# Performance work log

Hardware: AMD Instinct MI355X
Metric: run time of the kernel (lower is better)

Reference implementation:

```python
import jax, jax.numpy as jnp
import numpy as np

B, S, DIM = 2, 2048, 1024
N_HEAD, HEAD_DIM = 16, 64


def setup_inputs() -> dict:
    key = jax.random.key(0)
    k1, k2, k3, k4 = jax.random.split(key, 4)
    x = jax.random.normal(k1, (B, S, DIM), dtype=jnp.float32)
    # rotary table: cos/sin pairs, shape [S, head_dim//2, 2]
    half = HEAD_DIM // 2
    inv_freq = 1.0 / (10000.0 ** (jnp.arange(0, half, dtype=jnp.float32) / half))
    t = jnp.arange(S, dtype=jnp.float32)
    ang = t[:, None] * inv_freq[None, :]
    freqs_cis = jnp.stack([jnp.cos(ang), jnp.sin(ang)], axis=-1)  # [S, half, 2]
    # causal boolean mask [1,1,S,S] (True = attend)
    mask = jnp.tril(jnp.ones((S, S), dtype=bool))[None, None]
    wqkv = jax.random.normal(k2, (3 * DIM, DIM), dtype=jnp.float32) * (DIM ** -0.5)
    wo = jax.random.normal(k3, (DIM, DIM), dtype=jnp.float32) * (DIM ** -0.5)
    return {"x": x, "freqs_cis": freqs_cis, "mask": mask, "wqkv": wqkv, "wo": wo}


def apply_rotary_emb(x, freqs_cis):
    # x: [B, S, H, D]; freqs_cis: [S, D//2, 2]
    xs = x.reshape(*x.shape[:-1], -1, 2)  # [B,S,H,D//2,2]
    fc = freqs_cis[None, :, None, :, :]  # [1,S,1,D//2,2]
    xr, xi = xs[..., 0], xs[..., 1]
    cr, ci = fc[..., 0], fc[..., 1]
    out = jnp.stack([xr * cr - xi * ci, xi * cr + xr * ci], axis=-1)
    return out.reshape(x.shape)


def reference(x, freqs_cis, mask, wqkv, wo):
    bsz, seqlen, _ = x.shape
    qkv = jnp.einsum('bsd,ed->bse', x, wqkv)  # [B,S,3*dim]
    q, k, v = jnp.split(qkv, 3, axis=-1)
    q = q.reshape(bsz, seqlen, N_HEAD, HEAD_DIM)
    k = k.reshape(bsz, seqlen, N_HEAD, HEAD_DIM)
    v = v.reshape(bsz, seqlen, N_HEAD, HEAD_DIM)
    q = apply_rotary_emb(q, freqs_cis)
    k = apply_rotary_emb(k, freqs_cis)
    scale = HEAD_DIM ** -0.5
    scores = jnp.einsum('bqhd,bkhd->bhqk', q, k) * scale  # [B,H,S,S]
    scores = jnp.where(mask, scores, jnp.finfo(scores.dtype).min)
    attn = jax.nn.softmax(scores, axis=-1)
    y = jnp.einsum('bhqk,bkhd->bqhd', attn, v).reshape(bsz, seqlen, N_HEAD * HEAD_DIM)
    return jnp.einsum('bse,de->bsd', y, wo)
```

## Files before the change

kernel.cpp:

```cpp
#include <hip/hip_runtime.h>
#include <hip/hip_bf16.h>
#include <stdint.h>


typedef __attribute__((ext_vector_type(8))) __bf16 bf16x8;
typedef __attribute__((ext_vector_type(4))) float f32x4;

union B8 { uint4 u; bf16x8 v; unsigned short us[8]; };

static __device__ __forceinline__ float bf2f(unsigned short u) {
  union { unsigned int ui; float f; } x; x.ui = ((unsigned int)u) << 16; return x.f;
}
static __device__ __forceinline__ unsigned short f2bf(float f) {
  union { float f; unsigned int ui; } x; x.f = f;
  unsigned int r = x.ui + 0x7fffu + ((x.ui >> 16) & 1u);
  return (unsigned short)(r >> 16);
}
static __device__ __forceinline__ f32x4 mfma16(bf16x8 a, bf16x8 b, f32x4 c) {
  return __builtin_amdgcn_mfma_f32_16x16x32_bf16(a, b, c, 0, 0, 0);
}
#define AS1 __attribute__((address_space(1)))
#define AS3 __attribute__((address_space(3)))
static __device__ __forceinline__ void gload_lds16(const void* g, void* l) {
  __builtin_amdgcn_global_load_lds((const AS1 unsigned int*)g,
                                   (AS3 unsigned int*)l, 16, 0, 0);
}

__global__ __launch_bounds__(256) void cvt_all_kernel(
    const float* __restrict__ x, const float* __restrict__ wqkv,
    const float* __restrict__ wo,
    unsigned short* __restrict__ xb, unsigned short* __restrict__ wqkvb,
    unsigned short* __restrict__ wob) {
  int i = blockIdx.x * 256 + threadIdx.x;
  const float* src; unsigned short* dst; int off;
  if (i < 1048576)       { src = x;    dst = xb;    off = i; }
  else if (i < 1835008)  { src = wqkv; dst = wqkvb; off = i - 1048576; }
  else                   { src = wo;   dst = wob;   off = i - 1835008; }
  float4 f = ((const float4*)src)[off];
  ushort4 u;
  u.x = f2bf(f.x); u.y = f2bf(f.y); u.z = f2bf(f.z); u.w = f2bf(f.w);
  ((ushort4*)dst)[off] = u;
}

__global__ __launch_bounds__(256) void qkv_rope_kernel(
    const unsigned short* __restrict__ xb,
    const unsigned short* __restrict__ wqkvb,
    const float* __restrict__ freqs,
    unsigned short* __restrict__ Q,
    unsigned short* __restrict__ K,
    unsigned short* __restrict__ Vt)
{
  __shared__ __align__(16) unsigned short As[128 * 64];
  __shared__ __align__(16) unsigned short Bs[128 * 64];
  const int t = threadIdx.x;
  const int lane = t & 63, wv = t >> 6;
  const int c = lane & 15, quad = lane >> 4;
  const int wm = wv >> 1, wn = wv & 1;
  const int tm = blockIdx.x & 31, tn = blockIdx.x >> 5;
  const int m0 = tm * 128, n0 = tn * 128;

  f32x4 acc[4][4] = {};

  for (int k0 = 0; k0 < 1024; k0 += 64) {
    for (int r = 0; r < 4; ++r) {
      int cid = t + 256 * r;
      int row = cid >> 3, jc = cid & 7;
      int sc = jc ^ (row & 7);
      gload_lds16(xb    + (size_t)(m0 + row) * 1024 + k0 + sc * 8, (char*)As + cid * 16);
      gload_lds16(wqkvb + (size_t)(n0 + row) * 1024 + k0 + sc * 8, (char*)Bs + cid * 16);
    }
    __syncthreads();
    for (int ks = 0; ks < 2; ++ks) {
      bf16x8 a[4], b[4];
      for (int st = 0; st < 4; ++st) {
        int ra = wm * 64 + st * 16 + c;
        int sa = (ks * 4 + quad) ^ (ra & 7);
        a[st] = *(const bf16x8*)((const char*)As + ra * 128 + sa * 16);
        int rb = wn * 64 + st * 16 + c;
        int sb = (ks * 4 + quad) ^ (rb & 7);
        b[st] = *(const bf16x8*)((const char*)Bs + rb * 128 + sb * 16);
      }
      for (int sm = 0; sm < 4; ++sm)
        for (int sn = 0; sn < 4; ++sn)
          acc[sm][sn] = mfma16(a[sm], b[sn], acc[sm][sn]);
    }
    __syncthreads();
  }

  for (int sm = 0; sm < 4; ++sm) {
    for (int sn = 0; sn < 4; ++sn) {
      const int e = n0 + wn * 64 + sn * 16 + c;
      const int seg = e >> 10;
      const int eh = e & 1023;
      const int h = eh >> 6, d = eh & 63;
      for (int i = 0; i < 4; ++i) {
        const int m = m0 + wm * 64 + sm * 16 + quad * 4 + i;
        const int b_ = m >> 11, s_ = m & 2047;
        float v = acc[sm][sn][i];
        if (seg == 2) {
          Vt[((size_t)(b_ * 16 + h) * 64 + d) * 2048 + s_] = f2bf(v);
        } else {
          float partner = __shfl_xor(v, 1, 64);
          const int p = d >> 1;
          float cr = freqs[s_ * 64 + p * 2];
          float ci = freqs[s_ * 64 + p * 2 + 1];
          float outv = (d & 1) ? (v * cr + partner * ci) : (v * cr - partner * ci);
          unsigned short* dst = (seg == 0) ? Q : K;
          dst[((size_t)(b_ * 16 + h) * 2048 + s_) * 64 + d] = f2bf(outv);
        }
      }
    }
  }
}

struct QState {
  bf16x8 qf0, qf1;
  f32x4 o[4];
  float lp[4];
};

static __device__ __forceinline__ void attn_chunk(
    QState& st, const char* Ks, const char* Vs, float* myp,
    int c, int quad, int k0, int q0, bool diag)
{
  f32x4 sfr[4];
  for (int kc = 0; kc < 4; ++kc) {
    const int key = kc * 16 + c;
    const int s0 = quad ^ (key & 7), s1 = (4 + quad) ^ (key & 7);
    f32x4 sacc = {};
    sacc = mfma16(st.qf0, *(const bf16x8*)(Ks + key * 128 + s0 * 16), sacc);
    sacc = mfma16(st.qf1, *(const bf16x8*)(Ks + key * 128 + s1 * 16), sacc);
    sfr[kc] = sacc;
  }
  for (int i = 0; i < 4; ++i) {
    const int qrow = q0 + quad * 4 + i;
    float e[4];
    for (int kc = 0; kc < 4; ++kc) {
      float arg = fmaf(sfr[kc][i], 0.18033688f, -20.19773057f);
      if (diag && (k0 + kc * 16 + c > qrow)) arg = -1e30f;
      e[kc] = exp2f(arg);
    }
    st.lp[i] += (e[0] + e[1]) + (e[2] + e[3]);
    const int prow = (quad * 4 + i) * 68;
    myp[prow + c]      = e[0];
    myp[prow + 16 + c] = e[1];
    myp[prow + 32 + c] = e[2];
    myp[prow + 48 + c] = e[3];
  }
  bf16x8 pf[2];
  for (int sH = 0; sH < 2; ++sH) {
    const float* src = myp + c * 68 + sH * 32 + quad * 8;
    float4 f0 = *(const float4*)(src);
    float4 f1 = *(const float4*)(src + 4);
    B8 p;
    p.us[0] = f2bf(f0.x); p.us[1] = f2bf(f0.y);
    p.us[2] = f2bf(f0.z); p.us[3] = f2bf(f0.w);
    p.us[4] = f2bf(f1.x); p.us[5] = f2bf(f1.y);
    p.us[6] = f2bf(f1.z); p.us[7] = f2bf(f1.w);
    pf[sH] = p.v;
  }
  for (int ct = 0; ct < 4; ++ct) {
    const int d = ct * 16 + c;
    const int s0 = quad ^ (d & 7), s1 = (4 + quad) ^ (d & 7);
    st.o[ct] = mfma16(pf[0], *(const bf16x8*)(Vs + d * 128 + s0 * 16), st.o[ct]);
    st.o[ct] = mfma16(pf[1], *(const bf16x8*)(Vs + d * 128 + s1 * 16), st.o[ct]);
  }
}

__global__ __launch_bounds__(256) void attn_partial_kernel(
    const unsigned short* __restrict__ Q,
    const unsigned short* __restrict__ K,
    const unsigned short* __restrict__ Vt,
    unsigned short* __restrict__ Po,
    float* __restrict__ Pl)
{
  __shared__ __align__(16) unsigned short Ks[64 * 64];
  __shared__ __align__(16) unsigned short Vs[64 * 64];
  __shared__ __align__(16) float plds[4][16 * 68];
  const int t = threadIdx.x;
  const int lane = t & 63, wv = t >> 6;
  const int c = lane & 15, quad = lane >> 4;
  const int bh = blockIdx.x & 31;
  const int rest = blockIdx.x >> 5;
  const int j = rest >> 1, half = rest & 1;
  const int qA = j * 64 + wv * 16;
  const int qB = (31 - j) * 64 + wv * 16;

  const unsigned short* Qb = Q + (size_t)bh * (2048 * 64);
  const unsigned short* Kb = K + (size_t)bh * (2048 * 64);
  const unsigned short* Vb = Vt + (size_t)bh * (64 * 2048);

  QState A = {}, Bst = {};
  A.qf0 = *(const bf16x8*)(Qb + (qA + c) * 64 + quad * 8);
  A.qf1 = *(const bf16x8*)(Qb + (qA + c) * 64 + 32 + quad * 8);
  Bst.qf0 = *(const bf16x8*)(Qb + (qB + c) * 64 + quad * 8);
  Bst.qf1 = *(const bf16x8*)(Qb + (qB + c) * 64 + 32 + quad * 8);

  float* myp = plds[wv];
  const int ktmax = 31 - j;

  for (int kt = half; kt <= ktmax; kt += 2) {
    const int k0 = kt * 64;
    __syncthreads();
    for (int r = 0; r < 2; ++r) {
      int cid = t + 256 * r;
      int row = cid >> 3, jc = cid & 7;
      int sc = jc ^ (row & 7);
      gload_lds16(Kb + (size_t)(k0 + row) * 64 + sc * 8, (char*)Ks + cid * 16);
      gload_lds16(Vb + (size_t)row * 2048 + k0 + sc * 8, (char*)Vs + cid * 16);
    }
    __syncthreads();
    attn_chunk(Bst, (const char*)Ks, (const char*)Vs, myp, c, quad,
               k0, qB, kt == ktmax);
    if (kt <= j)
      attn_chunk(A, (const char*)Ks, (const char*)Vs, myp, c, quad,
                 k0, qA, kt == j);
  }

  unsigned short* Poh = Po + (size_t)half * (32 * 2048 * 64) + (size_t)bh * (2048 * 64);
  float* Plh = Pl + (size_t)half * (32 * 2048) + bh * 2048;
  for (int set = 0; set < 2; ++set) {
    QState& st = set ? Bst : A;
    const int q0 = set ? qB : qA;
    for (int i = 0; i < 4; ++i) {
      float l = st.lp[i];
      l += __shfl_xor(l, 1, 16);
      l += __shfl_xor(l, 2, 16);
      l += __shfl_xor(l, 4, 16);
      l += __shfl_xor(l, 8, 16);
      const int s = q0 + quad * 4 + i;
      for (int ct = 0; ct < 4; ++ct)
        Poh[(size_t)s * 64 + ct * 16 + c] = f2bf(st.o[ct][i]);
      if (c == 0) Plh[s] = l;
    }
  }
}

__global__ __launch_bounds__(256) void combine_kernel(
    const unsigned short* __restrict__ Po, const float* __restrict__ Pl,
    unsigned short* __restrict__ Yb)
{
  const int idx = blockIdx.x * 256 + threadIdx.x;
  const int bh = idx >> 14, rem = idx & 16383;
  const int s = rem >> 3, g = rem & 7;
  const size_t base = (size_t)bh * (2048 * 64) + (size_t)s * 64 + g * 8;
  B8 a, b;
  a.u = *(const uint4*)(Po + base);
  b.u = *(const uint4*)(Po + (size_t)(32 * 2048 * 64) + base);
  float l = Pl[bh * 2048 + s] + Pl[32 * 2048 + bh * 2048 + s];
  float inv = 1.0f / l;
  B8 y;
  for (int k = 0; k < 8; ++k)
    y.us[k] = f2bf((bf2f(a.us[k]) + bf2f(b.us[k])) * inv);
  const int b_ = bh >> 4, h = bh & 15;
  *(uint4*)(Yb + ((size_t)(b_ * 2048 + s)) * 1024 + h * 64 + g * 8) = y.u;
}

__global__ __launch_bounds__(256) void attn_kernel(
    const unsigned short* __restrict__ Q,
    const unsigned short* __restrict__ K,
    const unsigned short* __restrict__ Vt,
    unsigned short* __restrict__ Y)
{
  __shared__ __align__(16) unsigned short Ks[64 * 64];
  __shared__ __align__(16) unsigned short Vs[64 * 64];
  __shared__ __align__(16) float plds[4][16 * 68];
  const int t = threadIdx.x;
  const int lane = t & 63, wv = t >> 6;
  const int c = lane & 15, quad = lane >> 4;
  const int j = blockIdx.x >> 5, bh = blockIdx.x & 31;
  const int b = bh >> 4, h = bh & 15;
  const int qA = j * 64 + wv * 16;
  const int qB = (31 - j) * 64 + wv * 16;

  const unsigned short* Qb = Q + (size_t)bh * (2048 * 64);
  const unsigned short* Kb = K + (size_t)bh * (2048 * 64);
  const unsigned short* Vb = Vt + (size_t)bh * (64 * 2048);

  QState A = {}, Bst = {};
  A.qf0 = *(const bf16x8*)(Qb + (qA + c) * 64 + quad * 8);
  A.qf1 = *(const bf16x8*)(Qb + (qA + c) * 64 + 32 + quad * 8);
  Bst.qf0 = *(const bf16x8*)(Qb + (qB + c) * 64 + quad * 8);
  Bst.qf1 = *(const bf16x8*)(Qb + (qB + c) * 64 + 32 + quad * 8);

  const int nkt = 32 - j;
  float* myp = plds[wv];

  for (int kt = 0; kt < nkt; ++kt) {
    const int k0 = kt * 64;
    __syncthreads();
    for (int r = 0; r < 2; ++r) {
      int cid = t + 256 * r;
      int row = cid >> 3, jc = cid & 7;
      int sc = jc ^ (row & 7);
      gload_lds16(Kb + (size_t)(k0 + row) * 64 + sc * 8, (char*)Ks + cid * 16);
      gload_lds16(Vb + (size_t)row * 2048 + k0 + sc * 8, (char*)Vs + cid * 16);
    }
    __syncthreads();
    attn_chunk(Bst, (const char*)Ks, (const char*)Vs, myp, c, quad,
               k0, qB, kt == 31 - j);
    if (kt <= j)
      attn_chunk(A, (const char*)Ks, (const char*)Vs, myp, c, quad,
                 k0, qA, kt == j);
  }

  for (int set = 0; set < 2; ++set) {
    QState& st = set ? Bst : A;
    const int q0 = set ? qB : qA;
    for (int i = 0; i < 4; ++i) {
      float l = st.lp[i];
      l += __shfl_xor(l, 1, 16);
      l += __shfl_xor(l, 2, 16);
      l += __shfl_xor(l, 4, 16);
      l += __shfl_xor(l, 8, 16);
      float inv = 1.0f / l;
      const int s = q0 + quad * 4 + i;
      unsigned short* dst = Y + ((size_t)(b * 2048 + s)) * 1024 + h * 64;
      for (int ct = 0; ct < 4; ++ct)
        dst[ct * 16 + c] = f2bf(st.o[ct][i] * inv);
    }
  }
}

__global__ __launch_bounds__(256) void out_proj_kernel(
    const unsigned short* __restrict__ Y,
    const unsigned short* __restrict__ wob,
    float* __restrict__ out)
{
  __shared__ __align__(16) unsigned short As[64 * 64];
  __shared__ __align__(16) unsigned short Bs[64 * 64];
  const int t = threadIdx.x;
  const int lane = t & 63, wv = t >> 6;
  const int c = lane & 15, quad = lane >> 4;
  const int wm = wv >> 1, wn = wv & 1;
  const int tm = blockIdx.x & 63, tn = blockIdx.x >> 6;
  const int m0 = tm * 64, n0 = tn * 64;

  f32x4 acc[2][2] = {};

  for (int k0 = 0; k0 < 1024; k0 += 64) {
    for (int r = 0; r < 2; ++r) {
      int cid = t + 256 * r;
      int row = cid >> 3, jc = cid & 7;
      int sc = jc ^ (row & 7);
      gload_lds16(Y   + (size_t)(m0 + row) * 1024 + k0 + sc * 8, (char*)As + cid * 16);
      gload_lds16(wob + (size_t)(n0 + row) * 1024 + k0 + sc * 8, (char*)Bs + cid * 16);
    }
    __syncthreads();
    for (int ks = 0; ks < 2; ++ks) {
      bf16x8 a[2], b[2];
      for (int st = 0; st < 2; ++st) {
        int ra = wm * 32 + st * 16 + c;
        int sa = (ks * 4 + quad) ^ (ra & 7);
        a[st] = *(const bf16x8*)((const char*)As + ra * 128 + sa * 16);
        int rb = wn * 32 + st * 16 + c;
        int sb = (ks * 4 + quad) ^ (rb & 7);
        b[st] = *(const bf16x8*)((const char*)Bs + rb * 128 + sb * 16);
      }
      for (int sm = 0; sm < 2; ++sm)
        for (int sn = 0; sn < 2; ++sn)
          acc[sm][sn] = mfma16(a[sm], b[sn], acc[sm][sn]);
    }
    __syncthreads();
  }

  for (int sm = 0; sm < 2; ++sm)
    for (int sn = 0; sn < 2; ++sn)
      for (int i = 0; i < 4; ++i) {
        const int m = m0 + wm * 32 + sm * 16 + quad * 4 + i;
        const int e = n0 + wn * 32 + sn * 16 + c;
        out[(size_t)m * 1024 + e] = acc[sm][sn][i];
      }
}

extern "C" void kernel_launch(void* const* d_in, const int* in_sizes, int n_in,
                              void* d_out, int out_size, void* d_ws, size_t ws_size,
                              hipStream_t stream) {
  const float* x     = (const float*)d_in[0];
  const float* freqs = (const float*)d_in[1];
  const float* wqkv  = (const float*)d_in[3];
  const float* wo    = (const float*)d_in[4];
  float* out = (float*)d_out;

  const size_t BHSD = (size_t)2 * 16 * 2048 * 64;
  unsigned short* Q     = (unsigned short*)d_ws;
  unsigned short* K     = Q + BHSD;
  unsigned short* Vt    = K + BHSD;
  unsigned short* Yb    = Vt + BHSD;
  unsigned short* xb    = Yb + BHSD;
  unsigned short* wqkvb = xb + 4194304;
  unsigned short* wob   = wqkvb + 3145728;
  unsigned short* Po    = wob + 1048576;
  float*          Pl    = (float*)(Po + 2 * BHSD);

  const size_t need_fast =
      (size_t)((char*)(Pl + 2 * 32 * 2048) - (char*)d_ws);

  cvt_all_kernel<<<8192, 256, 0, stream>>>(x, wqkv, wo, xb, wqkvb, wob);
  qkv_rope_kernel<<<768, 256, 0, stream>>>(xb, wqkvb, freqs, Q, K, Vt);
  if (ws_size >= need_fast) {
    attn_partial_kernel<<<1024, 256, 0, stream>>>(Q, K, Vt, Po, Pl);
    combine_kernel<<<2048, 256, 0, stream>>>(Po, Pl, Yb);
  } else {
    attn_kernel<<<512, 256, 0, stream>>>(Q, K, Vt, Yb);
  }
  out_proj_kernel<<<1024, 256, 0, stream>>>(Yb, wob, out);
}
```

Before: 229.0 us.

## Use 32x32 MFMA in QKV GEMM, fuse split-KV combine into out-projection, double attention work per block

The QKV projection GEMM switches from 16x16x32 to 32x32x16 bf16 MFMA tiles, with a new lane mapping for the RoPE epilogue. The attention partial kernel now processes two query-block pairs per workgroup, halving the grid and reusing each loaded K/V tile across four query states. The separate combine kernel is removed: its normalise-and-sum of the two split-KV partials is folded into the A-tile load of a new out-projection kernel. This saves a launch and the round trip of the intermediate Y tensor, but the A operand is now loaded through registers rather than direct-to-LDS, and the attention grid has fewer, longer workgroups.

```diff
diff --git a/kernel.cpp b/kernel.cpp
--- a/kernel.cpp
+++ b/kernel.cpp
@@ -5,6 +5,7 @@
 
 typedef __attribute__((ext_vector_type(8))) __bf16 bf16x8;
 typedef __attribute__((ext_vector_type(4))) float f32x4;
+typedef __attribute__((ext_vector_type(16))) float f32x16;
 
 union B8 { uint4 u; bf16x8 v; unsigned short us[8]; };
 
@@ -18,6 +19,9 @@
 }
 static __device__ __forceinline__ f32x4 mfma16(bf16x8 a, bf16x8 b, f32x4 c) {
   return __builtin_amdgcn_mfma_f32_16x16x32_bf16(a, b, c, 0, 0, 0);
+}
+static __device__ __forceinline__ f32x16 mfma32(bf16x8 a, bf16x8 b, f32x16 c) {
+  return __builtin_amdgcn_mfma_f32_32x32x16_bf16(a, b, c, 0, 0, 0);
 }
 #define AS1 __attribute__((address_space(1)))
 #define AS3 __attribute__((address_space(3)))
@@ -54,12 +58,12 @@
   __shared__ __align__(16) unsigned short Bs[128 * 64];
   const int t = threadIdx.x;
   const int lane = t & 63, wv = t >> 6;
-  const int c = lane & 15, quad = lane >> 4;
+  const int l31 = lane & 31, lh = lane >> 5;
   const int wm = wv >> 1, wn = wv & 1;
   const int tm = blockIdx.x & 31, tn = blockIdx.x >> 5;
   const int m0 = tm * 128, n0 = tn * 128;
 
-  f32x4 acc[4][4] = {};
+  f32x16 acc[2][2] = {};
 
   for (int k0 = 0; k0 < 1024; k0 += 64) {
     for (int r = 0; r < 4; ++r) {
@@ -70,40 +74,38 @@
       gload_lds16(wqkvb + (size_t)(n0 + row) * 1024 + k0 + sc * 8, (char*)Bs + cid * 16);
     }
     __syncthreads();
-    for (int ks = 0; ks < 2; ++ks) {
-      bf16x8 a[4], b[4];
-      for (int st = 0; st < 4; ++st) {
-        int ra = wm * 64 + st * 16 + c;
-        int sa = (ks * 4 + quad) ^ (ra & 7);
-        a[st] = *(const bf16x8*)((const char*)As + ra * 128 + sa * 16);
-        int rb = wn * 64 + st * 16 + c;
-        int sb = (ks * 4 + quad) ^ (rb & 7);
-        b[st] = *(const bf16x8*)((const char*)Bs + rb * 128 + sb * 16);
-      }
-      for (int sm = 0; sm < 4; ++sm)
-        for (int sn = 0; sn < 4; ++sn)
-          acc[sm][sn] = mfma16(a[sm], b[sn], acc[sm][sn]);
-    }
-    __syncthreads();
-  }
-
-  for (int sm = 0; sm < 4; ++sm) {
-    for (int sn = 0; sn < 4; ++sn) {
-      const int e = n0 + wn * 64 + sn * 16 + c;
+    for (int kst = 0; kst < 4; ++kst) {
+      const int g = kst * 2 + lh;
+      bf16x8 a[2], b[2];
+      for (int s2 = 0; s2 < 2; ++s2) {
+        int ra = wm * 64 + s2 * 32 + l31;
+        a[s2] = *(const bf16x8*)((const char*)As + ra * 128 + (g ^ (ra & 7)) * 16);
+        int rb = wn * 64 + s2 * 32 + l31;
+        b[s2] = *(const bf16x8*)((const char*)Bs + rb * 128 + (g ^ (rb & 7)) * 16);
+      }
+      for (int sm = 0; sm < 2; ++sm)
+        for (int sn = 0; sn < 2; ++sn)
+          acc[sm][sn] = mfma32(a[sm], b[sn], acc[sm][sn]);
+    }
+    __syncthreads();
+  }
+
+  for (int sm = 0; sm < 2; ++sm) {
+    for (int sn = 0; sn < 2; ++sn) {
+      const int e = n0 + wn * 64 + sn * 32 + l31;
       const int seg = e >> 10;
       const int eh = e & 1023;
       const int h = eh >> 6, d = eh & 63;
-      for (int i = 0; i < 4; ++i) {
-        const int m = m0 + wm * 64 + sm * 16 + quad * 4 + i;
+      for (int r = 0; r < 16; ++r) {
+        const int m = m0 + wm * 64 + sm * 32 + (r & 3) + 8 * (r >> 2) + 4 * lh;
         const int b_ = m >> 11, s_ = m & 2047;
-        float v = acc[sm][sn][i];
+        float v = acc[sm][sn][r];
         if (seg == 2) {
           Vt[((size_t)(b_ * 16 + h) * 64 + d) * 2048 + s_] = f2bf(v);
         } else {
           float partner = __shfl_xor(v, 1, 64);
-          const int p = d >> 1;
-          float cr = freqs[s_ * 64 + p * 2];
-          float ci = freqs[s_ * 64 + p * 2 + 1];
+          float cr = freqs[s_ * 64 + (d & ~1)];
+          float ci = freqs[s_ * 64 + (d | 1)];
           float outv = (d & 1) ? (v * cr + partner * ci) : (v * cr - partner * ci);
           unsigned short* dst = (seg == 0) ? Q : K;
           dst[((size_t)(b_ * 16 + h) * 2048 + s_) * 64 + d] = f2bf(outv);
@@ -118,6 +120,12 @@
   f32x4 o[4];
   float lp[4];
 };
+
+static __device__ __forceinline__ void load_q(QState& st,
+    const unsigned short* Qb, int q0, int c, int quad) {
+  st.qf0 = *(const bf16x8*)(Qb + (q0 + c) * 64 + quad * 8);
+  st.qf1 = *(const bf16x8*)(Qb + (q0 + c) * 64 + 32 + quad * 8);
+}
 
 static __device__ __forceinline__ void attn_chunk(
     QState& st, const char* Ks, const char* Vs, float* myp,
@@ -167,6 +175,23 @@
   }
 }
 
+static __device__ __forceinline__ void write_state(
+    QState& st, int q0, int c, int quad,
+    unsigned short* Poh, float* Plh)
+{
+  for (int i = 0; i < 4; ++i) {
+    float l = st.lp[i];
+    l += __shfl_xor(l, 1, 16);
+    l += __shfl_xor(l, 2, 16);
+    l += __shfl_xor(l, 4, 16);
+    l += __shfl_xor(l, 8, 16);
+    const int s = q0 + quad * 4 + i;
+    for (int ct = 0; ct < 4; ++ct)
+      Poh[(size_t)s * 64 + ct * 16 + c] = f2bf(st.o[ct][i]);
+    if (c == 0) Plh[s] = l;
+  }
+}
+
 __global__ __launch_bounds__(256) void attn_partial_kernel(
     const unsigned short* __restrict__ Q,
     const unsigned short* __restrict__ K,
@@ -181,23 +206,24 @@
   const int lane = t & 63, wv = t >> 6;
   const int c = lane & 15, quad = lane >> 4;
   const int bh = blockIdx.x & 31;
-  const int rest = blockIdx.x >> 5;
-  const int j = rest >> 1, half = rest & 1;
-  const int qA = j * 64 + wv * 16;
-  const int qB = (31 - j) * 64 + wv * 16;
+  const int rr = blockIdx.x >> 5;
+  const int k8 = rr >> 1, half = rr & 1;
+  const int j0 = 2 * k8, j1 = 2 * k8 + 1;
+  const int qA0 = j0 * 64 + wv * 16,  qB0 = (31 - j0) * 64 + wv * 16;
+  const int qA1 = j1 * 64 + wv * 16,  qB1 = (31 - j1) * 64 + wv * 16;
 
   const unsigned short* Qb = Q + (size_t)bh * (2048 * 64);
   const unsigned short* Kb = K + (size_t)bh * (2048 * 64);
   const unsigned short* Vb = Vt + (size_t)bh * (64 * 2048);
 
-  QState A = {}, Bst = {};
-  A.qf0 = *(const bf16x8*)(Qb + (qA + c) * 64 + quad * 8);
-  A.qf1 = *(const bf16x8*)(Qb + (qA + c) * 64 + 32 + quad * 8);
-  Bst.qf0 = *(const bf16x8*)(Qb + (qB + c) * 64 + quad * 8);
-  Bst.qf1 = *(const bf16x8*)(Qb + (qB + c) * 64 + 32 + quad * 8);
+  QState A0 = {}, A1 = {}, B0 = {}, B1 = {};
+  load_q(A0, Qb, qA0, c, quad);
+  load_q(A1, Qb, qA1, c, quad);
+  load_q(B0, Qb, qB0, c, quad);
+  load_q(B1, Qb, qB1, c, quad);
 
   float* myp = plds[wv];
-  const int ktmax = 31 - j;
+  const int ktmax = 31 - j0;
 
   for (int kt = half; kt <= ktmax; kt += 2) {
     const int k0 = kt * 64;
@@ -210,50 +236,25 @@
       gload_lds16(Vb + (size_t)row * 2048 + k0 + sc * 8, (char*)Vs + cid * 16);
     }
     __syncthreads();
-    attn_chunk(Bst, (const char*)Ks, (const char*)Vs, myp, c, quad,
-               k0, qB, kt == ktmax);
-    if (kt <= j)
-      attn_chunk(A, (const char*)Ks, (const char*)Vs, myp, c, quad,
-                 k0, qA, kt == j);
+    attn_chunk(B0, (const char*)Ks, (const char*)Vs, myp, c, quad,
+               k0, qB0, kt == 31 - j0);
+    if (kt <= 31 - j1)
+      attn_chunk(B1, (const char*)Ks, (const char*)Vs, myp, c, quad,
+                 k0, qB1, kt == 31 - j1);
+    if (kt <= j1)
+      attn_chunk(A1, (const char*)Ks, (const char*)Vs, myp, c, quad,
+                 k0, qA1, kt == j1);
+    if (kt <= j0)
+      attn_chunk(A0, (const char*)Ks, (const char*)Vs, myp, c, quad,
+                 k0, qA0, kt == j0);
   }
 
   unsigned short* Poh = Po + (size_t)half * (32 * 2048 * 64) + (size_t)bh * (2048 * 64);
   float* Plh = Pl + (size_t)half * (32 * 2048) + bh * 2048;
-  for (int set = 0; set < 2; ++set) {
-    QState& st = set ? Bst : A;
-    const int q0 = set ? qB : qA;
-    for (int i = 0; i < 4; ++i) {
-      float l = st.lp[i];
-      l += __shfl_xor(l, 1, 16);
-      l += __shfl_xor(l, 2, 16);
-      l += __shfl_xor(l, 4, 16);
-      l += __shfl_xor(l, 8, 16);
-      const int s = q0 + quad * 4 + i;
-      for (int ct = 0; ct < 4; ++ct)
-        Poh[(size_t)s * 64 + ct * 16 + c] = f2bf(st.o[ct][i]);
-      if (c == 0) Plh[s] = l;
-    }
-  }
-}
-
-__global__ __launch_bounds__(256) void combine_kernel(
-    const unsigned short* __restrict__ Po, const float* __restrict__ Pl,
-    unsigned short* __restrict__ Yb)
-{
-  const int idx = blockIdx.x * 256 + threadIdx.x;
-  const int bh = idx >> 14, rem = idx & 16383;
-  const int s = rem >> 3, g = rem & 7;
-  const size_t base = (size_t)bh * (2048 * 64) + (size_t)s * 64 + g * 8;
-  B8 a, b;
-  a.u = *(const uint4*)(Po + base);
-  b.u = *(const uint4*)(Po + (size_t)(32 * 2048 * 64) + base);
-  float l = Pl[bh * 2048 + s] + Pl[32 * 2048 + bh * 2048 + s];
-  float inv = 1.0f / l;
-  B8 y;
-  for (int k = 0; k < 8; ++k)
-    y.us[k] = f2bf((bf2f(a.us[k]) + bf2f(b.us[k])) * inv);
-  const int b_ = bh >> 4, h = bh & 15;
-  *(uint4*)(Yb + ((size_t)(b_ * 2048 + s)) * 1024 + h * 64 + g * 8) = y.u;
+  write_state(A0, qA0, c, quad, Poh, Plh);
+  write_state(A1, qA1, c, quad, Poh, Plh);
+  write_state(B0, qB0, c, quad, Poh, Plh);
+  write_state(B1, qB1, c, quad, Poh, Plh);
 }
 
 __global__ __launch_bounds__(256) void attn_kernel(
@@ -278,10 +279,8 @@
   const unsigned short* Vb = Vt + (size_t)bh * (64 * 2048);
 
   QState A = {}, Bst = {};
-  A.qf0 = *(const bf16x8*)(Qb + (qA + c) * 64 + quad * 8);
-  A.qf1 = *(const bf16x8*)(Qb + (qA + c) * 64 + 32 + quad * 8);
-  Bst.qf0 = *(const bf16x8*)(Qb + (qB + c) * 64 + quad * 8);
-  Bst.qf1 = *(const bf16x8*)(Qb + (qB + c) * 64 + 32 + quad * 8);
+  load_q(A, Qb, qA, c, quad);
+  load_q(Bst, Qb, qB, c, quad);
 
   const int nkt = 32 - j;
   float* myp = plds[wv];
@@ -322,6 +321,68 @@
   }
 }
 
+__global__ __launch_bounds__(256) void out_proj_fused_kernel(
+    const unsigned short* __restrict__ Po, const float* __restrict__ Pl,
+    const unsigned short* __restrict__ wob,
+    float* __restrict__ out)
+{
+  __shared__ __align__(16) unsigned short As[64 * 64];
+  __shared__ __align__(16) unsigned short Bs[64 * 64];
+  const int t = threadIdx.x;
+  const int lane = t & 63, wv = t >> 6;
+  const int c = lane & 15, quad = lane >> 4;
+  const int wm = wv >> 1, wn = wv & 1;
+  const int tm = blockIdx.x & 63, tn = blockIdx.x >> 6;
+  const int m0 = tm * 64, n0 = tn * 64;
+
+  f32x4 acc[2][2] = {};
+
+  for (int k0 = 0; k0 < 1024; k0 += 64) {
+    const int h = k0 >> 6;
+    for (int r = 0; r < 2; ++r) {
+      int cid = t + 256 * r;
+      int row = cid >> 3, jc = cid & 7;
+      int sc = jc ^ (row & 7);
+      gload_lds16(wob + (size_t)(n0 + row) * 1024 + k0 + sc * 8, (char*)Bs + cid * 16);
+      const int m = m0 + row, b_ = m >> 11, s = m & 2047;
+      const int bh = b_ * 16 + h;
+      const size_t base = (size_t)bh * (2048 * 64) + (size_t)s * 64 + sc * 8;
+      B8 pa, pb, y;
+      pa.u = *(const uint4*)(Po + base);
+      pb.u = *(const uint4*)(Po + (size_t)(32 * 2048 * 64) + base);
+      float l = Pl[bh * 2048 + s] + Pl[32 * 2048 + bh * 2048 + s];
+      float inv = 1.0f / l;
+      for (int k = 0; k < 8; ++k)
+        y.us[k] = f2bf((bf2f(pa.us[k]) + bf2f(pb.us[k])) * inv);
+      *(uint4*)((char*)As + cid * 16) = y.u;
+    }
+    __syncthreads();
+    for (int ks = 0; ks < 2; ++ks) {
+      bf16x8 a[2], b[2];
+      for (int st = 0; st < 2; ++st) {
+        int ra = wm * 32 + st * 16 + c;
+        int sa = (ks * 4 + quad) ^ (ra & 7);
+        a[st] = *(const bf16x8*)((const char*)As + ra * 128 + sa * 16);
+        int rb = wn * 32 + st * 16 + c;
+        int sb = (ks * 4 + quad) ^ (rb & 7);
+        b[st] = *(const bf16x8*)((const char*)Bs + rb * 128 + sb * 16);
+      }
+      for (int sm = 0; sm < 2; ++sm)
+        for (int sn = 0; sn < 2; ++sn)
+          acc[sm][sn] = mfma16(a[sm], b[sn], acc[sm][sn]);
+    }
+    __syncthreads();
+  }
+
+  for (int sm = 0; sm < 2; ++sm)
+    for (int sn = 0; sn < 2; ++sn)
+      for (int i = 0; i < 4; ++i) {
+        const int m = m0 + wm * 32 + sm * 16 + quad * 4 + i;
+        const int e = n0 + wn * 32 + sn * 16 + c;
+        out[(size_t)m * 1024 + e] = acc[sm][sn][i];
+      }
+}
+
 __global__ __launch_bounds__(256) void out_proj_kernel(
     const unsigned short* __restrict__ Y,
     const unsigned short* __restrict__ wob,
@@ -399,10 +460,10 @@
   cvt_all_kernel<<<8192, 256, 0, stream>>>(x, wqkv, wo, xb, wqkvb, wob);
   qkv_rope_kernel<<<768, 256, 0, stream>>>(xb, wqkvb, freqs, Q, K, Vt);
   if (ws_size >= need_fast) {
-    attn_partial_kernel<<<1024, 256, 0, stream>>>(Q, K, Vt, Po, Pl);
-    combine_kernel<<<2048, 256, 0, stream>>>(Po, Pl, Yb);
+    attn_partial_kernel<<<512, 256, 0, stream>>>(Q, K, Vt, Po, Pl);
+    out_proj_fused_kernel<<<1024, 256, 0, stream>>>(Po, Pl, wob, out);
   } else {
     attn_kernel<<<512, 256, 0, stream>>>(Q, K, Vt, Yb);
-  }
-  out_proj_kernel<<<1024, 256, 0, stream>>>(Yb, wob, out);
-}
+    out_proj_kernel<<<1024, 256, 0, stream>>>(Yb, wob, out);
+  }
+}
```

Measured after the change: 248.9 us. +8.7%, slower.
